# Kernel tuning notes

Hardware: AMD Instinct MI355X
Metric: run time of the kernel (lower is better)

The kernel has to match this reference:

```python
import jax, jax.numpy as jnp
import numpy as np

H = 16      # n_head
DK = 64     # d_k = n_feat // n_head
EPS = 1e-5  # nn.LayerNorm default eps


def _layernorm(x, gamma, beta):
    # LayerNorm over the last (d_k) dim, matching nn.LayerNorm(d_k)
    mu = jnp.mean(x, axis=-1, keepdims=True)
    var = jnp.mean(jnp.square(x - mu), axis=-1, keepdims=True)
    return (x - mu) * jax.lax.rsqrt(var + EPS) * gamma + beta


def setup_inputs() -> dict:
    key = jax.random.key(0)
    ks = jax.random.split(key, 10)
    B, T, D = 4, 1024, 1024
    s = 0.02
    inp = {
        "query": jax.random.normal(ks[0], (B, T, D), dtype=jnp.float32),
        "key":   jax.random.normal(ks[1], (B, T, D), dtype=jnp.float32),
        "value": jax.random.normal(ks[2], (B, T, D), dtype=jnp.float32),
        "mask":  jax.random.randint(ks[3], (B, T, T), 0, 2).astype(bool),
        # projection weights (torch nn.Linear: y = x @ W.T + b)
        "Wq": jax.random.normal(ks[4], (D, D), dtype=jnp.float32) * s,
        "bq": jnp.zeros((D,), dtype=jnp.float32),
        "Wk": jax.random.normal(ks[5], (D, D), dtype=jnp.float32) * s,
        "bk": jnp.zeros((D,), dtype=jnp.float32),
        "Wv": jax.random.normal(ks[6], (D, D), dtype=jnp.float32) * s,
        "bv": jnp.zeros((D,), dtype=jnp.float32),
        "Wo": jax.random.normal(ks[7], (D, D), dtype=jnp.float32) * s,
        "bo": jnp.zeros((D,), dtype=jnp.float32),
        # per-head LayerNorm params over d_k
        "q_gamma": jnp.ones((DK,), dtype=jnp.float32),
        "q_beta":  jnp.zeros((DK,), dtype=jnp.float32),
        "k_gamma": jnp.ones((DK,), dtype=jnp.float32),
        "k_beta":  jnp.zeros((DK,), dtype=jnp.float32),
    }
    return inp


def reference(query, key, value, mask, Wq, bq, Wk, bk, Wv, bv, Wo, bo,
              q_gamma, q_beta, k_gamma, k_beta):
    B, Tq, D = query.shape
    Tk = key.shape[1]
    # forward_qkv: project, split heads, QK-LayerNorm
    q = (query @ Wq.T + bq).reshape(B, Tq, H, DK)
    k = (key   @ Wk.T + bk).reshape(B, Tk, H, DK)
    q = _layernorm(q, q_gamma, q_beta).transpose(0, 2, 1, 3)  # (B,H,Tq,dk)
    k = _layernorm(k, k_gamma, k_beta).transpose(0, 2, 1, 3)  # (B,H,Tk,dk)
    v = (value @ Wv.T + bv).reshape(B, Tk, H, DK).transpose(0, 2, 1, 3)
    # scores scaled by sqrt(d_k)
    scores = jnp.einsum('bhqd,bhkd->bhqk', q, k) / jnp.sqrt(jnp.float32(DK))
    m = mask[:, None]  # (B,1,Tq,Tk) broadcast over heads
    scores = jnp.where(m, jnp.float32(-10000.0), scores)
    attn = jax.nn.softmax(scores, axis=-1)
    attn = jnp.where(m, jnp.float32(0.0), attn)
    # dropout is identity (p=0.0, eval)
    x = jnp.einsum('bhqk,bhkd->bhqd', attn, v)
    x = x.transpose(0, 2, 1, 3).reshape(B, Tq, H * DK)
    return x @ Wo.T + bo
```

## Files before the change

kernel.cpp:

```cpp
#include <hip/hip_runtime.h>
#include <cstdint>
#include <cstddef>

typedef _Float16 half8  __attribute__((ext_vector_type(8)));
typedef _Float16 half4v __attribute__((ext_vector_type(4)));
typedef float    f32x4  __attribute__((ext_vector_type(4)));

__device__ __forceinline__ f32x4 fzero4() {
  f32x4 v; v[0] = v[1] = v[2] = v[3] = 0.0f; return v;
}

__device__ __forceinline__ void gload16(const void* g, void* l) {
  __builtin_amdgcn_global_load_lds(
      (const __attribute__((address_space(1))) unsigned int*)g,
      (__attribute__((address_space(3))) unsigned int*)l, 16, 0, 0);
}

#define MFMA(a, b, c) __builtin_amdgcn_mfma_f32_16x16x32_f16(a, b, c, 0, 0, 0)
#define EXP2(x) __builtin_amdgcn_exp2f(x)

__device__ __forceinline__ float row16_sum(float x) {
#define STEP_(N)                                                         \
  {                                                                      \
    int t_ = __builtin_amdgcn_update_dpp(0, __float_as_int(x), 0x120 | N, \
                                         0xf, 0xf, true);                \
    x = x + __int_as_float(t_);                                          \
  }
  STEP_(8) STEP_(4) STEP_(2) STEP_(1)
#undef STEP_
  return x;
}

struct PrepArgs {
  const float* src[7];
  _Float16*    dst[7];
  const int*   mask;
  unsigned long long* mbits;
};

__global__ __launch_bounds__(256) void prep_kernel(PrepArgs a) {
  const int z = blockIdx.y;
  const int nthr = gridDim.x * blockDim.x;
  const int t0 = blockIdx.x * blockDim.x + threadIdx.x;
  if (z < 3) {
    const float4* __restrict__ s = (const float4*)a.src[z];
    half4v* __restrict__ d = (half4v*)a.dst[z];
    float4 v[8];
#pragma unroll
    for (int k = 0; k < 8; ++k) v[k] = s[t0 + k * nthr];
#pragma unroll
    for (int k = 0; k < 8; ++k) {
      half4v h;
      h[0] = (_Float16)v[k].x; h[1] = (_Float16)v[k].y;
      h[2] = (_Float16)v[k].z; h[3] = (_Float16)v[k].w;
      d[t0 + k * nthr] = h;
    }
  } else if (z < 7) {
    const float4* __restrict__ s = (const float4*)a.src[z];
    half4v* __restrict__ d = (half4v*)a.dst[z];
    float4 v[2];
#pragma unroll
    for (int k = 0; k < 2; ++k) v[k] = s[t0 + k * nthr];
#pragma unroll
    for (int k = 0; k < 2; ++k) {
      half4v h;
      h[0] = (_Float16)v[k].x; h[1] = (_Float16)v[k].y;
      h[2] = (_Float16)v[k].z; h[3] = (_Float16)v[k].w;
      d[t0 + k * nthr] = h;
    }
  } else {
    const int* __restrict__ src = a.mask;
    const unsigned char* __restrict__ s8 = (const unsigned char*)src;
    unsigned long long* __restrict__ dst = a.mbits;
    const int lane = threadIdx.x & 63;
    unsigned probe = 0;
#pragma unroll
    for (int e = 0; e < 16; ++e) probe |= s8[4 * (lane * 16 + e) + 1];
    const bool isbool = __any(probe != 0);

    const int wv = blockIdx.x * 4 + (threadIdx.x >> 6);
    if (!isbool) {
      const int4* __restrict__ s4 = (const int4*)src;
      int4 mv[8];
#pragma unroll
      for (int i = 0; i < 8; ++i) {
        const int unit = wv * 8 + i;
        const int row = unit >> 2, kg = unit & 3;
        mv[i] = s4[row * 256 + kg * 64 + lane];
      }
#pragma unroll
      for (int i = 0; i < 8; ++i) {
        const int unit = wv * 8 + i;
        unsigned long long w0 = __ballot(mv[i].x != 0);
        unsigned long long w1 = __ballot(mv[i].y != 0);
        unsigned long long w2 = __ballot(mv[i].z != 0);
        unsigned long long w3 = __ballot(mv[i].w != 0);
        if (lane == 0) {
          unsigned long long* p = dst + (size_t)unit * 4;
          p[0] = w0; p[1] = w1; p[2] = w2; p[3] = w3;
        }
      }
    } else {
      for (int i = 0; i < 8; ++i) {
        const int unit = wv * 8 + i;
        const int row = unit >> 2, kg = unit & 3;
#pragma unroll
        for (int c = 0; c < 4; ++c) {
          int m = s8[(size_t)row * 1024 + kg * 256 + lane * 4 + c];
          unsigned long long bw = __ballot(m != 0);
          if (lane == 0) dst[(size_t)unit * 4 + c] = bw;
        }
      }
    }
  }
}

#define SM_SCALE 0.18033688011112042f

__global__ __launch_bounds__(256) void proj_kernel(
    const _Float16* __restrict__ q16, const _Float16* __restrict__ k16,
    const _Float16* __restrict__ v16, const _Float16* __restrict__ w16,
    const float* __restrict__ bq, const float* __restrict__ bk,
    const float* __restrict__ bv,
    const float* __restrict__ qg, const float* __restrict__ qbt,
    const float* __restrict__ kg, const float* __restrict__ kbt,
    _Float16* __restrict__ Qln, _Float16* __restrict__ Kln,
    _Float16* __restrict__ VT) {
  __shared__ _Float16 As[128 * 64];
  __shared__ _Float16 Bs[128 * 64];

  const int tid = threadIdx.x;
  const int w = tid >> 6, lane = tid & 63, g = lane >> 4, l15 = lane & 15;
  const int flat = blockIdx.x;
  const int swz = (flat & 7) * 96 + (flat >> 3);
  const int bn = swz & 7;
  const int bm = (swz >> 3) & 31;
  const int z = swz >> 8;

  const _Float16* A = (z == 0) ? q16 : ((z == 1) ? k16 : v16);
  const _Float16* W = w16 + (size_t)z * (1024 * 1024);
  const float* bias = (z == 0) ? bq : ((z == 1) ? bk : bv);

  const int wr = w >> 1, wc = w & 1;
  const int srow = (w << 3) + (lane >> 3);
  const int csw = ((lane & 7) ^ (lane >> 3)) << 3;
  const int rsw = (l15 & 7) << 3;

  f32x4 acc[4][4];
#pragma unroll
  for (int i = 0; i < 4; ++i)
#pragma unroll
    for (int j = 0; j < 4; ++j) acc[i][j] = fzero4();

#define PROJ_STAGE(KT)                                                      \
  _Pragma("unroll") for (int r = 0; r < 4; ++r) {                           \
    const int row = r * 32 + srow;                                          \
    gload16(A + (size_t)(bm * 128 + row) * 1024 + (KT)*64 + csw,            \
            &As[(r * 32 + (w << 3)) * 64]);                                 \
    gload16(W + (size_t)(bn * 128 + row) * 1024 + (KT)*64 + csw,            \
            &Bs[(r * 32 + (w << 3)) * 64]);                                 \
  }

#define PROJ_COMP()                                                         \
  _Pragma("unroll") for (int kk = 0; kk < 2; ++kk) {                        \
    half8 a[4], b[4];                                                       \
    _Pragma("unroll") for (int mi = 0; mi < 4; ++mi) a[mi] =                \
        *(const half8*)&As[(wr * 64 + mi * 16 + l15) * 64 +                 \
                           ((kk * 32 + g * 8) ^ rsw)];                      \
    _Pragma("unroll") for (int nj = 0; nj < 4; ++nj) b[nj] =                \
        *(const half8*)&Bs[(wc * 64 + nj * 16 + l15) * 64 +                 \
                           ((kk * 32 + g * 8) ^ rsw)];                      \
    __builtin_amdgcn_s_setprio(1);                                          \
    _Pragma("unroll") for (int mi = 0; mi < 4; ++mi)                        \
        _Pragma("unroll") for (int nj = 0; nj < 4; ++nj) acc[mi][nj] =      \
            MFMA(a[mi], b[nj], acc[mi][nj]);                                \
    __builtin_amdgcn_s_setprio(0);                                          \
  }

  for (int kt = 0; kt < 16; ++kt) {
    PROJ_STAGE(kt)
    asm volatile("s_waitcnt vmcnt(0)" ::: "memory");
    __syncthreads();
    PROJ_COMP()
    __syncthreads();
  }
#undef PROJ_COMP
#undef PROJ_STAGE

  const int colbase = bn * 128 + wc * 64;
  const int h = colbase >> 6;
  const int rowbase = bm * 128 + wr * 64;

  float biasv[4];
#pragma unroll
  for (int nj = 0; nj < 4; ++nj) biasv[nj] = bias[colbase + nj * 16 + l15];

  if (z < 2) {
    const float* gamma = (z == 0) ? qg : kg;
    const float* beta = (z == 0) ? qbt : kbt;
    const float sc = (z == 0) ? SM_SCALE : 1.0f;
    _Float16* dst = (z == 0) ? Qln : Kln;
    float gam[4], bet[4];
#pragma unroll
    for (int nj = 0; nj < 4; ++nj) {
      gam[nj] = gamma[nj * 16 + l15] * sc;
      bet[nj] = beta[nj * 16 + l15] * sc;
    }
#pragma unroll
    for (int mi = 0; mi < 4; ++mi) {
#pragma unroll
      for (int j = 0; j < 4; ++j) {
        float vals[4], s = 0.f, s2 = 0.f;
#pragma unroll
        for (int nj = 0; nj < 4; ++nj) {
          float v = acc[mi][nj][j] + biasv[nj];
          vals[nj] = v; s += v; s2 += v * v;
        }
        s = row16_sum(s);
        s2 = row16_sum(s2);
        const float mu = s * (1.0f / 64.0f);
        const float var = s2 * (1.0f / 64.0f) - mu * mu;
        const float rs = rsqrtf(var + 1e-5f);
        const int r = rowbase + mi * 16 + g * 4 + j;
        const int b = r >> 10, t = r & 1023;
        _Float16* drow = dst + ((size_t)((b * 16 + h) * 1024 + t)) * 64;
#pragma unroll
        for (int nj = 0; nj < 4; ++nj)
          drow[nj * 16 + l15] =
              (_Float16)((vals[nj] - mu) * rs * gam[nj] + bet[nj]);
      }
    }
  } else {
#pragma unroll
    for (int mi = 0; mi < 4; ++mi) {
      const int r0 = rowbase + mi * 16 + g * 4;
      const int b = r0 >> 10, t0 = r0 & 1023;
#pragma unroll
      for (int nj = 0; nj < 4; ++nj) {
        const int dk = nj * 16 + l15;
        half4v pk;
#pragma unroll
        for (int j = 0; j < 4; ++j)
          pk[j] = (_Float16)(acc[mi][nj][j] + biasv[nj]);
        *(half4v*)&VT[((size_t)((b * 16 + h) * 64 + dk)) * 1024 + t0] = pk;
      }
    }
  }
}

#define PSTR 76

__global__ __launch_bounds__(512) void attn_kernel(
    const _Float16* __restrict__ Qln, const _Float16* __restrict__ Kln,
    const _Float16* __restrict__ VT,
    const unsigned long long* __restrict__ mbits, _Float16* __restrict__ X) {
  __shared__ _Float16 PQ[128 * PSTR];
  __shared__ _Float16 Ks[2][64 * 64];
  __shared__ _Float16 Vs[2][64 * 64];
  __shared__ unsigned long long Mb2[2][128 * 4];

  const int tid = threadIdx.x;
  const int w = tid >> 6, lane = tid & 63, g = lane >> 4, l15 = lane & 15;
  const int qt = blockIdx.y;
  const int bh = blockIdx.x;
  const int b = bh >> 4, h = bh & 15;

  const int lr8 = lane >> 3;
  const int csw = ((lane & 7) ^ lr8) << 3;

  const _Float16* Qb = Qln + (size_t)bh * 65536;
  const _Float16* Kb = Kln + (size_t)bh * 65536;
  const _Float16* Vb = VT + (size_t)bh * 65536;
  const unsigned long long* mbb = mbits + (size_t)b * 16384;

#define MB_STAGE(M, BUF)                                                     \
  if (w < 4)                                                                 \
    gload16(mbb + (size_t)(qt * 128 + w * 32 + (lane >> 1)) * 16 + (M)*4 +   \
                (lane & 1) * 2,                                              \
            &Mb2[BUF][(w * 32) * 4]);

  gload16(Qb + (size_t)(qt * 128 + w * 16 + lr8) * 64 + csw, &PQ[(w * 16) * 64]);
  gload16(Qb + (size_t)(qt * 128 + w * 16 + 8 + lr8) * 64 + csw,
          &PQ[(w * 16 + 8) * 64]);
  gload16(Kb + (size_t)(w * 8 + lr8) * 64 + csw, &Ks[0][(w * 8) * 64]);
  gload16(Vb + (size_t)(w * 8 + lr8) * 1024 + csw, &Vs[0][(w * 8) * 64]);
  MB_STAGE(0, 0)
  asm volatile("s_waitcnt vmcnt(0)" ::: "memory");
  __syncthreads();

  const int rsw = (l15 & 7) << 3;
  half8 qf[2];
#pragma unroll
  for (int kk = 0; kk < 2; ++kk)
    qf[kk] = *(const half8*)&PQ[(w * 16 + l15) * 64 + ((kk * 32 + g * 8) ^ rsw)];
  asm volatile("s_waitcnt lgkmcnt(0)" ::: "memory");
  __syncthreads();

  f32x4 o[4];
  float lsum[4];
#pragma unroll
  for (int dn = 0; dn < 4; ++dn) o[dn] = fzero4();
#pragma unroll
  for (int j = 0; j < 4; ++j) lsum[j] = 0.f;

#define ATTN_TILE(KT, CUR, NXT, PF)                                          \
  {                                                                          \
    if (PF) {                                                                \
      gload16(Kb + (size_t)(((KT) + 1) * 64 + w * 8 + lr8) * 64 + csw,       \
              &Ks[NXT][(w * 8) * 64]);                                       \
      gload16(Vb + (size_t)(w * 8 + lr8) * 1024 + ((KT) + 1) * 64 + csw,     \
              &Vs[NXT][(w * 8) * 64]);                                       \
    }                                                                        \
    if ((((KT) & 3) == 0) && (((KT) >> 2) < 3)) {                            \
      MB_STAGE(((KT) >> 2) + 1, (((KT) >> 2) + 1) & 1)                       \
    }                                                                        \
    f32x4 s[4];                                                              \
    _Pragma("unroll") for (int nj = 0; nj < 4; ++nj) s[nj] = fzero4();       \
    _Pragma("unroll") for (int kk = 0; kk < 2; ++kk) {                       \
      half8 qv = qf[kk];                                                     \
      __builtin_amdgcn_s_setprio(1);                                         \
      _Pragma("unroll") for (int nj = 0; nj < 4; ++nj) {                     \
        half8 kf = *(const half8*)&Ks[CUR][(nj * 16 + l15) * 64 +            \
                                          ((kk * 32 + g * 8) ^ rsw)];        \
        s[nj] = MFMA(qv, kf, s[nj]);                                         \
      }                                                                      \
      __builtin_amdgcn_s_setprio(0);                                         \
    }                                                                        \
    _Pragma("unroll") for (int j = 0; j < 4; ++j) {                          \
      const int lrow = w * 16 + g * 4 + j;                                   \
      const unsigned long long mw =                                          \
          Mb2[((KT) >> 2) & 1][lrow * 4 + (l15 & 3)];                        \
      const int bb = ((KT) & 3) * 16 + (l15 >> 2);                           \
      const float p0 = ((mw >> bb) & 1) ? 0.f : EXP2(s[0][j]);               \
      const float p1 = ((mw >> (bb + 4)) & 1) ? 0.f : EXP2(s[1][j]);         \
      const float p2 = ((mw >> (bb + 8)) & 1) ? 0.f : EXP2(s[2][j]);         \
      const float p3 = ((mw >> (bb + 12)) & 1) ? 0.f : EXP2(s[3][j]);        \
      PQ[lrow * PSTR + 0 + l15] = (_Float16)p0;                              \
      PQ[lrow * PSTR + 16 + l15] = (_Float16)p1;                             \
      PQ[lrow * PSTR + 32 + l15] = (_Float16)p2;                             \
      PQ[lrow * PSTR + 48 + l15] = (_Float16)p3;                             \
      lsum[j] += (p0 + p1) + (p2 + p3);                                      \
    }                                                                        \
    _Pragma("unroll") for (int kk = 0; kk < 2; ++kk) {                       \
      half8 pa = *(const half8*)&PQ[(w * 16 + l15) * PSTR + kk * 32 + g * 8];\
      __builtin_amdgcn_s_setprio(1);                                         \
      _Pragma("unroll") for (int dn = 0; dn < 4; ++dn) {                     \
        half8 vf = *(const half8*)&Vs[CUR][(dn * 16 + l15) * 64 +            \
                                           ((kk * 32 + g * 8) ^ rsw)];       \
        o[dn] = MFMA(pa, vf, o[dn]);                                         \
      }                                                                      \
      __builtin_amdgcn_s_setprio(0);                                         \
    }                                                                        \
    if (PF) {                                                                \
      asm volatile("s_waitcnt vmcnt(0)" ::: "memory");                       \
      __syncthreads();                                                       \
    }                                                                        \
  }

  for (int kt = 0; kt < 16; kt += 2) {
    ATTN_TILE(kt, 0, 1, true);
    ATTN_TILE(kt + 1, 1, 0, (kt + 1) < 15);
  }
#undef ATTN_TILE
#undef MB_STAGE

#pragma unroll
  for (int j = 0; j < 4; ++j) {
    const int t = qt * 128 + w * 16 + g * 4 + j;
    const float inv = 1.0f / row16_sum(lsum[j]);
    _Float16* xrow = X + ((size_t)(b * 1024 + t)) * 1024 + h * 64;
#pragma unroll
    for (int dn = 0; dn < 4; ++dn)
      xrow[dn * 16 + l15] = (_Float16)(o[dn][j] * inv);
  }
}

__global__ __launch_bounds__(256) void ogemm_kernel(
    const _Float16* __restrict__ Xin, const _Float16* __restrict__ Wo16,
    const float* __restrict__ bo, float* __restrict__ out) {
  __shared__ _Float16 As[2][128 * 64];
  __shared__ _Float16 Bs[2][64 * 64];

  const int tid = threadIdx.x;
  const int w = tid >> 6, lane = tid & 63, g = lane >> 4, l15 = lane & 15;
  const int flat = blockIdx.x;
  const int swz = (flat & 7) * 64 + (flat >> 3);
  const int bn = swz & 15;
  const int bm = swz >> 4;
  const int wr = w >> 1, wc = w & 1;
  const int srow = (w << 3) + (lane >> 3);
  const int lr8 = lane >> 3;
  const int csw = ((lane & 7) ^ lr8) << 3;
  const int rsw = (l15 & 7) << 3;

  f32x4 acc[4][2];
#pragma unroll
  for (int i = 0; i < 4; ++i)
#pragma unroll
    for (int j = 0; j < 2; ++j) acc[i][j] = fzero4();

#define OG_STAGE(KT, BUF)                                                   \
  {                                                                         \
    _Pragma("unroll") for (int r = 0; r < 4; ++r) {                         \
      gload16(Xin + (size_t)(bm * 128 + r * 32 + srow) * 1024 + (KT)*64 +   \
                  csw,                                                      \
              &As[BUF][(r * 32 + (w << 3)) * 64]);                          \
    }                                                                       \
    _Pragma("unroll") for (int c = 0; c < 2; ++c) {                         \
      gload16(Wo16 + (size_t)(bn * 64 + w * 16 + c * 8 + lr8) * 1024 +      \
                  (KT)*64 + csw,                                            \
              &Bs[BUF][(w * 16 + c * 8) * 64]);                             \
    }                                                                       \
  }

#define OG_TILE(KT, CUR, NXT, PF)                                           \
  {                                                                         \
    if (PF) { OG_STAGE((KT) + 1, NXT) }                                     \
    _Pragma("unroll") for (int kk = 0; kk < 2; ++kk) {                      \
      half8 a[4], b[2];                                                     \
      _Pragma("unroll") for (int mi = 0; mi < 4; ++mi) a[mi] =              \
          *(const half8*)&As[CUR][(wr * 64 + mi * 16 + l15) * 64 +          \
                                  ((kk * 32 + g * 8) ^ rsw)];               \
      _Pragma("unroll") for (int nj = 0; nj < 2; ++nj) b[nj] =              \
          *(const half8*)&Bs[CUR][(wc * 32 + nj * 16 + l15) * 64 +          \
                                  ((kk * 32 + g * 8) ^ rsw)];               \
      __builtin_amdgcn_s_setprio(1);                                        \
      _Pragma("unroll") for (int mi = 0; mi < 4; ++mi)                      \
          _Pragma("unroll") for (int nj = 0; nj < 2; ++nj) acc[mi][nj] =    \
              MFMA(a[mi], b[nj], acc[mi][nj]);                              \
      __builtin_amdgcn_s_setprio(0);                                        \
    }                                                                       \
    if (PF) {                                                               \
      asm volatile("s_waitcnt vmcnt(0)" ::: "memory");                      \
      __syncthreads();                                                      \
    }                                                                       \
  }

  OG_STAGE(0, 0)
  asm volatile("s_waitcnt vmcnt(0)" ::: "memory");
  __syncthreads();
  for (int kt = 0; kt < 16; kt += 2) {
    OG_TILE(kt, 0, 1, true);
    OG_TILE(kt + 1, 1, 0, (kt + 1) < 15);
  }
#undef OG_TILE
#undef OG_STAGE

  const int colbase = bn * 64 + wc * 32;
  const int rowbase = bm * 128 + wr * 64;
  float biasv[2];
#pragma unroll
  for (int nj = 0; nj < 2; ++nj) biasv[nj] = bo[colbase + nj * 16 + l15];
#pragma unroll
  for (int mi = 0; mi < 4; ++mi)
#pragma unroll
    for (int nj = 0; nj < 2; ++nj)
#pragma unroll
      for (int j = 0; j < 4; ++j) {
        const int r = rowbase + mi * 16 + g * 4 + j;
        out[(size_t)r * 1024 + colbase + nj * 16 + l15] =
            acc[mi][nj][j] + biasv[nj];
      }
}

extern "C" void kernel_launch(void* const* d_in, const int* in_sizes, int n_in,
                              void* d_out, int out_size, void* d_ws,
                              size_t ws_size, hipStream_t stream) {
  const float* query = (const float*)d_in[0];
  const float* key = (const float*)d_in[1];
  const float* value = (const float*)d_in[2];
  const int* mask = (const int*)d_in[3];
  const float* Wq = (const float*)d_in[4];
  const float* bq = (const float*)d_in[5];
  const float* Wk = (const float*)d_in[6];
  const float* bk = (const float*)d_in[7];
  const float* Wv = (const float*)d_in[8];
  const float* bv = (const float*)d_in[9];
  const float* Wo = (const float*)d_in[10];
  const float* bo = (const float*)d_in[11];
  const float* qg = (const float*)d_in[12];
  const float* qb = (const float*)d_in[13];
  const float* kg = (const float*)d_in[14];
  const float* kb = (const float*)d_in[15];
  float* out = (float*)d_out;

  const size_t M4 = (size_t)4 * 1024 * 1024;
  const size_t M1 = (size_t)1024 * 1024;
  _Float16* q16 = (_Float16*)d_ws;
  _Float16* k16 = q16 + M4;
  _Float16* v16 = k16 + M4;
  _Float16* w16 = v16 + M4;
  _Float16* Qln = w16 + M4;
  _Float16* Kln = Qln + M4;
  _Float16* VTp = Kln + M4;
  _Float16* X = q16;
  unsigned long long* mbits = (unsigned long long*)(VTp + M4);

  PrepArgs pa;
  pa.src[0] = query; pa.src[1] = key; pa.src[2] = value;
  pa.src[3] = Wq; pa.src[4] = Wk; pa.src[5] = Wv; pa.src[6] = Wo;
  pa.dst[0] = q16; pa.dst[1] = k16; pa.dst[2] = v16;
  pa.dst[3] = w16; pa.dst[4] = w16 + M1; pa.dst[5] = w16 + 2 * M1;
  pa.dst[6] = w16 + 3 * M1;
  pa.mask = mask;
  pa.mbits = mbits;

  prep_kernel<<<dim3(512, 8), 256, 0, stream>>>(pa);
  proj_kernel<<<dim3(768), 256, 0, stream>>>(
      q16, k16, v16, w16, bq, bk, bv, qg, qb, kg, kb, Qln, Kln, VTp);
  attn_kernel<<<dim3(64, 8), 512, 0, stream>>>(Qln, Kln, VTp, mbits, X);
  ogemm_kernel<<<dim3(512), 256, 0, stream>>>(X, w16 + 3 * M1, bo, out);
}
```

Baseline: 115.4 us.

## Fuse fp32-to-fp16 activation conversion into projection GEMM loads

Result: no change. 113.7 us (-1.5%).

```diff
diff --git a/kernel.cpp b/kernel.cpp
--- a/kernel.cpp
+++ b/kernel.cpp
@@ -32,8 +32,8 @@
 }
 
 struct PrepArgs {
-  const float* src[7];
-  _Float16*    dst[7];
+  const float* wsrc[4];
+  _Float16*    wdst[4];
   const int*   mask;
   unsigned long long* mbits;
 };
@@ -42,22 +42,9 @@
   const int z = blockIdx.y;
   const int nthr = gridDim.x * blockDim.x;
   const int t0 = blockIdx.x * blockDim.x + threadIdx.x;
-  if (z < 3) {
-    const float4* __restrict__ s = (const float4*)a.src[z];
-    half4v* __restrict__ d = (half4v*)a.dst[z];
-    float4 v[8];
-#pragma unroll
-    for (int k = 0; k < 8; ++k) v[k] = s[t0 + k * nthr];
-#pragma unroll
-    for (int k = 0; k < 8; ++k) {
-      half4v h;
-      h[0] = (_Float16)v[k].x; h[1] = (_Float16)v[k].y;
-      h[2] = (_Float16)v[k].z; h[3] = (_Float16)v[k].w;
-      d[t0 + k * nthr] = h;
-    }
-  } else if (z < 7) {
-    const float4* __restrict__ s = (const float4*)a.src[z];
-    half4v* __restrict__ d = (half4v*)a.dst[z];
+  if (z < 4) {
+    const float4* __restrict__ s = (const float4*)a.wsrc[z];
+    half4v* __restrict__ d = (half4v*)a.wdst[z];
     float4 v[2];
 #pragma unroll
     for (int k = 0; k < 2; ++k) v[k] = s[t0 + k * nthr];
@@ -118,15 +105,15 @@
 #define SM_SCALE 0.18033688011112042f
 
 __global__ __launch_bounds__(256) void proj_kernel(
-    const _Float16* __restrict__ q16, const _Float16* __restrict__ k16,
-    const _Float16* __restrict__ v16, const _Float16* __restrict__ w16,
+    const float* __restrict__ query, const float* __restrict__ key,
+    const float* __restrict__ value, const _Float16* __restrict__ w16,
     const float* __restrict__ bq, const float* __restrict__ bk,
     const float* __restrict__ bv,
     const float* __restrict__ qg, const float* __restrict__ qbt,
     const float* __restrict__ kg, const float* __restrict__ kbt,
     _Float16* __restrict__ Qln, _Float16* __restrict__ Kln,
     _Float16* __restrict__ VT) {
-  __shared__ _Float16 As[128 * 64];
+  __shared__ float    As[128 * 64];
   __shared__ _Float16 Bs[128 * 64];
 
   const int tid = threadIdx.x;
@@ -137,7 +124,7 @@
   const int bm = (swz >> 3) & 31;
   const int z = swz >> 8;
 
-  const _Float16* A = (z == 0) ? q16 : ((z == 1) ? k16 : v16);
+  const float* Af = (z == 0) ? query : ((z == 1) ? key : value);
   const _Float16* W = w16 + (size_t)z * (1024 * 1024);
   const float* bias = (z == 0) ? bq : ((z == 1) ? bk : bv);
 
@@ -146,6 +133,10 @@
   const int csw = ((lane & 7) ^ (lane >> 3)) << 3;
   const int rsw = (l15 & 7) << 3;
 
+  const int arowin = w * 4 + (lane >> 4);
+  const int acsw = (((lane & 15) ^ ((arowin & 7) << 1)) << 2);
+  const int arsw = (l15 & 7) << 1;
+
   f32x4 acc[4][4];
 #pragma unroll
   for (int i = 0; i < 4; ++i)
@@ -153,20 +144,32 @@
     for (int j = 0; j < 4; ++j) acc[i][j] = fzero4();
 
 #define PROJ_STAGE(KT)                                                      \
+  _Pragma("unroll") for (int c = 0; c < 8; ++c) {                           \
+    gload16(Af + (size_t)(bm * 128 + c * 16 + arowin) * 1024 + (KT)*64 +    \
+                acsw,                                                       \
+            &As[(c * 16 + w * 4) * 64]);                                    \
+  }                                                                         \
   _Pragma("unroll") for (int r = 0; r < 4; ++r) {                           \
-    const int row = r * 32 + srow;                                          \
-    gload16(A + (size_t)(bm * 128 + row) * 1024 + (KT)*64 + csw,            \
-            &As[(r * 32 + (w << 3)) * 64]);                                 \
-    gload16(W + (size_t)(bn * 128 + row) * 1024 + (KT)*64 + csw,            \
+    gload16(W + (size_t)(bn * 128 + r * 32 + srow) * 1024 + (KT)*64 + csw,  \
             &Bs[(r * 32 + (w << 3)) * 64]);                                 \
   }
 
 #define PROJ_COMP()                                                         \
   _Pragma("unroll") for (int kk = 0; kk < 2; ++kk) {                        \
     half8 a[4], b[4];                                                       \
-    _Pragma("unroll") for (int mi = 0; mi < 4; ++mi) a[mi] =                \
-        *(const half8*)&As[(wr * 64 + mi * 16 + l15) * 64 +                 \
-                           ((kk * 32 + g * 8) ^ rsw)];                      \
+    _Pragma("unroll") for (int mi = 0; mi < 4; ++mi) {                      \
+      const int arow = (wr * 64 + mi * 16 + l15) * 64;                      \
+      const int s0 = (kk * 8 + g * 2) ^ arsw;                               \
+      const int s1 = (kk * 8 + g * 2 + 1) ^ arsw;                           \
+      f32x4 lo = *(const f32x4*)&As[arow + s0 * 4];                         \
+      f32x4 hi = *(const f32x4*)&As[arow + s1 * 4];                         \
+      half8 av;                                                             \
+      av[0] = (_Float16)lo[0]; av[1] = (_Float16)lo[1];                     \
+      av[2] = (_Float16)lo[2]; av[3] = (_Float16)lo[3];                     \
+      av[4] = (_Float16)hi[0]; av[5] = (_Float16)hi[1];                     \
+      av[6] = (_Float16)hi[2]; av[7] = (_Float16)hi[3];                     \
+      a[mi] = av;                                                           \
+    }                                                                       \
     _Pragma("unroll") for (int nj = 0; nj < 4; ++nj) b[nj] =                \
         *(const half8*)&Bs[(wc * 64 + nj * 16 + l15) * 64 +                 \
                            ((kk * 32 + g * 8) ^ rsw)];                      \
@@ -486,28 +489,24 @@
 
   const size_t M4 = (size_t)4 * 1024 * 1024;
   const size_t M1 = (size_t)1024 * 1024;
-  _Float16* q16 = (_Float16*)d_ws;
-  _Float16* k16 = q16 + M4;
-  _Float16* v16 = k16 + M4;
-  _Float16* w16 = v16 + M4;
-  _Float16* Qln = w16 + M4;
-  _Float16* Kln = Qln + M4;
-  _Float16* VTp = Kln + M4;
-  _Float16* X = q16;
-  unsigned long long* mbits = (unsigned long long*)(VTp + M4);
+  _Float16* base = (_Float16*)d_ws;
+  _Float16* X = base;
+  _Float16* w16 = base + 3 * M4;
+  _Float16* Qln = base + 4 * M4;
+  _Float16* Kln = base + 5 * M4;
+  _Float16* VTp = base + 6 * M4;
+  unsigned long long* mbits = (unsigned long long*)(base + 7 * M4);
 
   PrepArgs pa;
-  pa.src[0] = query; pa.src[1] = key; pa.src[2] = value;
-  pa.src[3] = Wq; pa.src[4] = Wk; pa.src[5] = Wv; pa.src[6] = Wo;
-  pa.dst[0] = q16; pa.dst[1] = k16; pa.dst[2] = v16;
-  pa.dst[3] = w16; pa.dst[4] = w16 + M1; pa.dst[5] = w16 + 2 * M1;
-  pa.dst[6] = w16 + 3 * M1;
+  pa.wsrc[0] = Wq; pa.wsrc[1] = Wk; pa.wsrc[2] = Wv; pa.wsrc[3] = Wo;
+  pa.wdst[0] = w16; pa.wdst[1] = w16 + M1; pa.wdst[2] = w16 + 2 * M1;
+  pa.wdst[3] = w16 + 3 * M1;
   pa.mask = mask;
   pa.mbits = mbits;
 
-  prep_kernel<<<dim3(512, 8), 256, 0, stream>>>(pa);
+  prep_kernel<<<dim3(512, 5), 256, 0, stream>>>(pa);
   proj_kernel<<<dim3(768), 256, 0, stream>>>(
-      q16, k16, v16, w16, bq, bk, bv, qg, qb, kg, kb, Qln, Kln, VTp);
+      query, key, value, w16, bq, bk, bv, qg, qb, kg, kb, Qln, Kln, VTp);
   attn_kernel<<<dim3(64, 8), 512, 0, stream>>>(Qln, Kln, VTp, mbits, X);
   ogemm_kernel<<<dim3(512), 256, 0, stream>>>(X, w16 + 3 * M1, bo, out);
 }
```
